# Kernel optimization log

Measured on AMD Instinct MI355X. Metric: run time of the kernel, lower is better.

Reference implementation:

```python
import jax, jax.numpy as jnp
import numpy as np

B, T, N = 64, 128, 64   # batch, win_size, input_size (= node_num)
H, E, K, CS = 64, 128, 7, 8  # hidden_size, embed_size, kernel_size, control_size
NEG_SLOPE = 0.2


def _p(key, shape, scale=0.05):
    return scale * jax.random.normal(key, shape, dtype=jnp.float32)


def setup_inputs() -> dict:
    key = jax.random.key(0)
    ks = jax.random.split(key, 32)
    inp = {
        "x": jax.random.normal(ks[0], (B, T, N), dtype=jnp.float32),
        "y": jax.random.normal(ks[1], (B, T, CS), dtype=jnp.float32),
        # Conv1d(N -> N, kernel K)
        "conv_w": _p(ks[2], (N, N, K)),
        "conv_b": _p(ks[3], (N,)),
        # rnn_enc GRU: input N -> hidden H
        "We_ih": _p(ks[4], (3 * H, N)), "We_hh": _p(ks[5], (3 * H, H)),
        "be_ih": _p(ks[6], (3 * H,)), "be_hh": _p(ks[7], (3 * H,)),
        # MP_GAT linears
        "Ww": _p(ks[8], (E, 2 * T)), "bw": _p(ks[9], (E,)),
        "Wa": _p(ks[10], (1, E)), "ba": _p(ks[11], (1,)),
        # encoder GRU: input H+N -> H
        "Wm_ih": _p(ks[12], (3 * H, H + N)), "Wm_hh": _p(ks[13], (3 * H, H)),
        "bm_ih": _p(ks[14], (3 * H,)), "bm_hh": _p(ks[15], (3 * H,)),
        # rnn_dec GRU: input H -> H
        "Wd_ih": _p(ks[16], (3 * H, H)), "Wd_hh": _p(ks[17], (3 * H, H)),
        "bd_ih": _p(ks[18], (3 * H,)), "bd_hh": _p(ks[19], (3 * H,)),
        # fc_dec: H -> N
        "W_dec": _p(ks[20], (N, H)), "b_dec": _p(ks[21], (N,)),
        # fc_pred: Linear(H,N), ReLU, Linear(N,N)
        "W_p1": _p(ks[22], (N, H)), "b_p1": _p(ks[23], (N,)),
        "W_p2": _p(ks[24], (N, N)), "b_p2": _p(ks[25], (N,)),
    }
    return inp


def gru_seq(x_seq, Wih, Whh, bih, bhh):
    """torch nn.GRU (batch_first, h0=0). x_seq: [B,T,in] -> [B,T,H]."""
    gi = jnp.einsum('bti,gi->btg', x_seq, Wih) + bih  # [B,T,3H] (precompute input proj)
    h0 = jnp.zeros((x_seq.shape[0], Whh.shape[1]), x_seq.dtype)

    def step(h, gi_t):
        gh = h @ Whh.T + bhh
        i_r, i_z, i_n = jnp.split(gi_t, 3, axis=-1)
        h_r, h_z, h_n = jnp.split(gh, 3, axis=-1)
        r = jax.nn.sigmoid(i_r + h_r)
        z = jax.nn.sigmoid(i_z + h_z)
        n = jnp.tanh(i_n + r * h_n)
        h_new = (1.0 - z) * n + z * h
        return h_new, h_new

    _, hs = jax.lax.scan(step, h0, jnp.swapaxes(gi, 0, 1))
    return jnp.swapaxes(hs, 0, 1)


def _forward(x, y, conv_w, conv_b, We_ih, We_hh, be_ih, be_hh, Ww, bw, Wa, ba,
             Wm_ih, Wm_hh, bm_ih, bm_hh, Wd_ih, Wd_hh, bd_ih, bd_hh,
             W_dec, b_dec, W_p1, b_p1, W_p2, b_p2):
    # ---- CNN: pad 'same' + Conv1d + SELU. x: [B,T,N] -> channels first [B,N,T]
    pad = (K - 1) // 2
    xc = jnp.swapaxes(x, 1, 2)
    c = jax.lax.conv_general_dilated(xc, conv_w, (1,), [(pad, pad)],
                                     dimension_numbers=('NCH', 'OIH', 'NCH'))
    c = jax.nn.selu(c + conv_b[None, :, None])  # [B,N,T]
    c_btn = jnp.swapaxes(c, 1, 2)               # [B,T,N]

    # ---- rnn_enc GRU over time
    h_out = gru_seq(c_btn, We_ih, We_hh, be_ih, be_hh)  # [B,T,H]

    # ---- MP_GAT on c (v: [B, node, seq] = [B,N,T])
    v = c
    vi = jnp.broadcast_to(v[:, :, None, :], (B, N, N, T))
    vj = jnp.broadcast_to(v[:, None, :, :], (B, N, N, T))
    v_cat = jnp.concatenate([vi, vj], axis=-1)          # [B,N,N,2T]
    x_w = jax.nn.leaky_relu(jnp.einsum('bijt,et->bije', v_cat, Ww) + bw, NEG_SLOPE)
    e = (jnp.einsum('bije,oe->bijo', x_w, Wa) + ba)[..., 0]  # [B,N,N]
    attention = jax.nn.softmax(e, axis=2)
    # dropout is identity in eval mode
    h_mp = jax.nn.sigmoid(jnp.einsum('bij,bjt->bit', attention, v))  # [B,N,T]
    h_mp = jnp.swapaxes(h_mp, 1, 2)                      # [B,T,N]

    # ---- encoder / decoder GRUs (dropout = identity in eval)
    h_cat = jnp.concatenate([h_out, h_mp], axis=2)       # [B,T,H+N]
    h_enc = gru_seq(h_cat, Wm_ih, Wm_hh, bm_ih, bm_hh)
    h_dec = gru_seq(h_enc, Wd_ih, Wd_hh, bd_ih, bd_hh)

    recon = h_dec @ W_dec.T + b_dec                      # [B,T,N]
    p = jax.nn.relu(h_dec[:, 0, :] @ W_p1.T + b_p1)
    pred = p @ W_p2.T + b_p2                             # [B,N]
    return recon, pred


def reference(x, y, conv_w, conv_b, We_ih, We_hh, be_ih, be_hh, Ww, bw, Wa, ba,
              Wm_ih, Wm_hh, bm_ih, bm_hh, Wd_ih, Wd_hh, bd_ih, bd_hh,
              W_dec, b_dec, W_p1, b_p1, W_p2, b_p2):
    return _forward(x, y, conv_w, conv_b, We_ih, We_hh, be_ih, be_hh, Ww, bw, Wa, ba,
                    Wm_ih, Wm_hh, bm_ih, bm_hh, Wd_ih, Wd_hh, bd_ih, bd_hh,
                    W_dec, b_dec, W_p1, b_p1, W_p2, b_p2)
```

## Files before the change

### kernel.cpp

```cpp
#include <hip/hip_runtime.h>
#include <math.h>

#define BB 64
#define TT 128
#define NN 64
#define HH 64
#define EE 128
#define KK 7
#define GG 192

typedef _Float16 half2_t __attribute__((ext_vector_type(2)));

__device__ __forceinline__ float sigmoidf_(float x){ return 1.f/(1.f+expf(-x)); }
__device__ __forceinline__ float fsig_(float x){
  return __builtin_amdgcn_rcpf(1.f + __builtin_amdgcn_exp2f(-1.44269504f * x));
}
__device__ __forceinline__ float ftanh_(float x){
  return fmaf(-2.f, __builtin_amdgcn_rcpf(1.f + __builtin_amdgcn_exp2f(2.88539008f * x)), 1.f);
}

#define PIPE_BARRIER() asm volatile("s_waitcnt lgkmcnt(0)\ns_barrier" ::: "memory")
#define LGKM0() asm volatile("s_waitcnt lgkmcnt(0)" ::: "memory")

__device__ __forceinline__ void loadrow_(float* d, const float* src){
  const float4* p = (const float4*)src;
  #pragma unroll
  for (int i = 0; i < 16; ++i) {
    float4 v = p[i];
    d[4*i] = v.x; d[4*i+1] = v.y; d[4*i+2] = v.z; d[4*i+3] = v.w;
  }
}
__device__ __forceinline__ void loadroww_(half2_t* d, const float* src){
  const float4* p = (const float4*)src;
  #pragma unroll
  for (int i = 0; i < 16; ++i) {
    float4 v = p[i];
    d[2*i]   = half2_t{(_Float16)v.x, (_Float16)v.y};
    d[2*i+1] = half2_t{(_Float16)v.z, (_Float16)v.w};
  }
}
__device__ __forceinline__ void mv6_(const _Float16* xs, const _Float16* ys,
    const half2_t* wxa, const half2_t* wxb, const half2_t* wxc,
    const half2_t* wya, const half2_t* wyb, const half2_t* wyc,
    float& a0, float& a1, float& a2, float& r0, float& r1, float& r2){
  const float4* x4 = (const float4*)xs;
  const float4* y4 = (const float4*)ys;
  #pragma unroll
  for (int ch = 0; ch < 8; ++ch) {
    float4 xv = x4[ch], yv = y4[ch];
    const half2_t* xq = (const half2_t*)&xv;
    const half2_t* yq = (const half2_t*)&yv;
    #pragma unroll
    for (int k = 0; k < 4; ++k) {
      int i = 4 * ch + k;
      a0 = __builtin_amdgcn_fdot2(xq[k], wxa[i], a0, false);
      a1 = __builtin_amdgcn_fdot2(xq[k], wxb[i], a1, false);
      a2 = __builtin_amdgcn_fdot2(xq[k], wxc[i], a2, false);
      r0 = __builtin_amdgcn_fdot2(yq[k], wya[i], r0, false);
      r1 = __builtin_amdgcn_fdot2(yq[k], wyb[i], r1, false);
      r2 = __builtin_amdgcn_fdot2(yq[k], wyc[i], r2, false);
    }
  }
}
__device__ __forceinline__ void mv3_(const _Float16* xs,
    const half2_t* wxa, const half2_t* wxb, const half2_t* wxc,
    float& a0, float& a1, float& a2){
  const float4* x4 = (const float4*)xs;
  #pragma unroll
  for (int ch = 0; ch < 8; ++ch) {
    float4 xv = x4[ch];
    const half2_t* xq = (const half2_t*)&xv;
    #pragma unroll
    for (int k = 0; k < 4; ++k) {
      int i = 4 * ch + k;
      a0 = __builtin_amdgcn_fdot2(xq[k], wxa[i], a0, false);
      a1 = __builtin_amdgcn_fdot2(xq[k], wxb[i], a1, false);
      a2 = __builtin_amdgcn_fdot2(xq[k], wxc[i], a2, false);
    }
  }
}

__global__ void conv_selu_kernel(const float* __restrict__ x, const float* __restrict__ w,
                                 const float* __restrict__ bias,
                                 float* __restrict__ c_nt, float* __restrict__ c_btn) {
  const int og = blockIdx.x, b = blockIdx.y, t = threadIdx.x;
  const int o0 = og * 8;
  __shared__ __align__(16) float xs[NN][TT + 1];
  __shared__ __align__(16) float ws[NN * KK][8];
  for (int idx = t; idx < TT * NN; idx += 128) {
    int tt = idx >> 6, nn = idx & 63;
    xs[nn][tt] = x[(size_t)(b * TT + tt) * NN + nn];
  }
  for (int idx = t; idx < NN * KK * 8; idx += 128) {
    int oo = idx & 7, ik = idx >> 3;
    ws[ik][oo] = w[(size_t)(o0 + oo) * (NN * KK) + ik];
  }
  __syncthreads();
  float acc[8];
  #pragma unroll
  for (int oo = 0; oo < 8; ++oo) acc[oo] = bias[o0 + oo];
  for (int i = 0; i < NN; ++i) {
    #pragma unroll
    for (int k = 0; k < KK; ++k) {
      int tt = t + k - 3;
      if (tt >= 0 && tt < TT) {
        float xv = xs[i][tt];
        const float* wp = &ws[i * KK + k][0];
        float4 w0 = *(const float4*)wp;
        float4 w1 = *(const float4*)(wp + 4);
        acc[0] += xv * w0.x; acc[1] += xv * w0.y; acc[2] += xv * w0.z; acc[3] += xv * w0.w;
        acc[4] += xv * w1.x; acc[5] += xv * w1.y; acc[6] += xv * w1.z; acc[7] += xv * w1.w;
      }
    }
  }
  const float alpha = 1.6732632423543772f, scale = 1.0507009873554805f;
  #pragma unroll
  for (int oo = 0; oo < 8; ++oo) {
    float a = acc[oo];
    float r = a > 0.f ? scale * a : scale * alpha * expm1f(a);
    int o = o0 + oo;
    c_nt[((size_t)b * NN + o) * TT + t] = r;
    c_btn[((size_t)b * TT + t) * NN + o] = r;
  }
}

__global__ void s12_kernel(const float* __restrict__ c_nt, const float* __restrict__ Ww,
                           float* __restrict__ s1, float* __restrict__ s2) {
  const int m0 = blockIdx.x * 16, col = threadIdx.x;
  __shared__ __align__(16) float ins[16][TT];
  for (int idx = col; idx < 16 * TT; idx += 128) {
    int r = idx >> 7, k = idx & 127;
    ins[r][k] = c_nt[(size_t)(m0 + r) * TT + k];
  }
  __syncthreads();
  const float* w1 = Ww + (size_t)col * (2 * TT);
  const float* w2 = w1 + TT;
  float acc1[16], acc2[16];
  #pragma unroll
  for (int r = 0; r < 16; ++r) { acc1[r] = 0.f; acc2[r] = 0.f; }
  #pragma unroll 2
  for (int k = 0; k < TT; k += 4) {
    float4 wv1 = *(const float4*)(w1 + k);
    float4 wv2 = *(const float4*)(w2 + k);
    #pragma unroll
    for (int r = 0; r < 16; ++r) {
      float4 iv = *(const float4*)&ins[r][k];
      acc1[r] += iv.x * wv1.x + iv.y * wv1.y + iv.z * wv1.z + iv.w * wv1.w;
      acc2[r] += iv.x * wv2.x + iv.y * wv2.y + iv.z * wv2.z + iv.w * wv2.w;
    }
  }
  #pragma unroll
  for (int r = 0; r < 16; ++r) {
    s1[(size_t)(m0 + r) * EE + col] = acc1[r];
    s2[(size_t)(m0 + r) * EE + col] = acc2[r];
  }
}

__global__ void gat_kernel(const float* __restrict__ s1, const float* __restrict__ s2,
                           const float* __restrict__ bw, const float* __restrict__ Wa,
                           const float* __restrict__ ba, const float* __restrict__ c_nt,
                           float* __restrict__ hmp) {
  const int it = blockIdx.x, b = blockIdx.y, tid = threadIdx.x;
  const int i0 = it * 16;
  __shared__ float s2s[NN][EE + 1];
  __shared__ float s1b[16][EE];
  __shared__ float cs[NN][TT + 1];
  __shared__ float was[EE];
  __shared__ float att[16][NN];
  for (int idx = tid; idx < NN * EE; idx += 256) {
    int j = idx >> 7, e = idx & 127;
    s2s[j][e] = s2[((size_t)b * NN + j) * EE + e] + bw[e];
  }
  for (int idx = tid; idx < 16 * EE; idx += 256) {
    int r = idx >> 7, e = idx & 127;
    s1b[r][e] = s1[((size_t)b * NN + i0 + r) * EE + e];
  }
  for (int idx = tid; idx < NN * TT; idx += 256) {
    int j = idx >> 7, t = idx & 127;
    cs[j][t] = c_nt[((size_t)b * NN + j) * TT + t];
  }
  if (tid < EE) was[tid] = Wa[tid];
  __syncthreads();
  const int wv = tid >> 6, j = tid & 63;
  #pragma unroll
  for (int pass = 0; pass < 4; ++pass) {
    const int il = pass * 4 + wv;
    float acc = 0.f;
    #pragma unroll 8
    for (int e = 0; e < EE; ++e) {
      float v = s1b[il][e] + s2s[j][e];
      v = v > 0.f ? v : 0.2f * v;
      acc += was[e] * v;
    }
    float ej = acc + ba[0];
    float mx = ej;
    for (int off = 32; off >= 1; off >>= 1) mx = fmaxf(mx, __shfl_xor(mx, off));
    float ex = __builtin_amdgcn_exp2f(1.44269504f * (ej - mx));
    float sm = ex;
    for (int off = 32; off >= 1; off >>= 1) sm += __shfl_xor(sm, off);
    att[il][j] = ex / sm;
  }
  __syncthreads();
  for (int o = tid; o < 16 * TT; o += 256) {
    int il = o >> 7, t = o & 127;
    float acc = 0.f;
    #pragma unroll 8
    for (int jj = 0; jj < NN; ++jj) acc += att[il][jj] * cs[jj][t];
    hmp[((size_t)b * TT + t) * NN + i0 + il] = sigmoidf_(acc);
  }
}

#define K4 4
__global__ __launch_bounds__(256, 1)
void fused_chain4k(const float* __restrict__ c_btn, const float* __restrict__ hmp,
                   const float* __restrict__ We_ih, const float* __restrict__ be_ih,
                   const float* __restrict__ We_hh, const float* __restrict__ be_hh,
                   const float* __restrict__ Wm_ih, const float* __restrict__ bm_ih,
                   const float* __restrict__ Wm_hh, const float* __restrict__ bm_hh,
                   const float* __restrict__ Wd_ih, const float* __restrict__ bd_ih,
                   const float* __restrict__ Wd_hh, const float* __restrict__ bd_hh,
                   const float* __restrict__ W_dec, const float* __restrict__ b_dec,
                   const float* __restrict__ W_p1, const float* __restrict__ b_p1,
                   const float* __restrict__ W_p2, const float* __restrict__ b_p2,
                   float* __restrict__ recon, float* __restrict__ pred) {
  const int b = blockIdx.x, tid = threadIdx.x, wid = tid >> 6, g = tid & 63;
  __shared__ __align__(16) _Float16 cbuf[2][K4][HH], mbuf[2][K4][HH];
  __shared__ __align__(16) _Float16 h1h[2][K4][HH], h2h[2][K4][HH], h3h[2][K4][HH];
  __shared__ __align__(16) float q2[2][K4][GG], h3f[2][K4][HH];
  __shared__ __align__(16) float h0s[HH], ps[HH];

  {
    _Float16* z1 = &h1h[0][0][0];
    _Float16* z2 = &h2h[0][0][0];
    _Float16* z3 = &h3h[0][0][0];
    _Float16* z4 = &cbuf[0][0][0];
    _Float16* z5 = &mbuf[0][0][0];
    for (int idx = tid; idx < 2 * K4 * HH; idx += 256) {
      z1[idx] = (_Float16)0.f; z2[idx] = (_Float16)0.f; z3[idx] = (_Float16)0.f;
      z4[idx] = (_Float16)0.f; z5[idx] = (_Float16)0.f;
    }
    float* zf = &h3f[0][0][0];
    for (int idx = tid; idx < 2 * K4 * HH; idx += 256) zf[idx] = 0.f;
    float* zq = &q2[0][0][0];
    for (int idx = tid; idx < 2 * K4 * GG; idx += 256) zq[idx] = 0.f;
  }

  half2_t wxa[32], wxb[32], wxc[32];
  half2_t wya[32], wyb[32], wyc[32];
  float wdec[64];
  float b0 = 0.f, b1 = 0.f, b2 = 0.f, e0 = 0.f, e1 = 0.f, e2 = 0.f, bdc = 0.f;
  if (wid == 0) {
    loadroww_(wxa, We_ih + (size_t)g * HH);
    loadroww_(wxb, We_ih + (size_t)(g + 64) * HH);
    loadroww_(wxc, We_ih + (size_t)(g + 128) * HH);
    loadroww_(wya, We_hh + (size_t)g * HH);
    loadroww_(wyb, We_hh + (size_t)(g + 64) * HH);
    loadroww_(wyc, We_hh + (size_t)(g + 128) * HH);
    b0 = be_ih[g]; b1 = be_ih[64 + g]; b2 = be_ih[128 + g];
    e0 = be_hh[g]; e1 = be_hh[64 + g]; e2 = be_hh[128 + g];
  } else if (wid == 1) {
    loadroww_(wxa, Wm_ih + (size_t)g * 128);
    loadroww_(wxb, Wm_ih + (size_t)(g + 64) * 128);
    loadroww_(wxc, Wm_ih + (size_t)(g + 128) * 128);
    loadroww_(wya, Wm_ih + (size_t)g * 128 + 64);
    loadroww_(wyb, Wm_ih + (size_t)(g + 64) * 128 + 64);
    loadroww_(wyc, Wm_ih + (size_t)(g + 128) * 128 + 64);
    b0 = bm_ih[g]; b1 = bm_ih[64 + g]; b2 = bm_ih[128 + g];
  } else if (wid == 2) {
    loadroww_(wxa, Wm_hh + (size_t)g * HH);
    loadroww_(wxb, Wm_hh + (size_t)(g + 64) * HH);
    loadroww_(wxc, Wm_hh + (size_t)(g + 128) * HH);
    loadrow_(wdec, W_dec + (size_t)g * HH);
    b0 = bm_hh[g]; b1 = bm_hh[64 + g]; b2 = bm_hh[128 + g];
    bdc = b_dec[g];
  } else {
    loadroww_(wxa, Wd_ih + (size_t)g * HH);
    loadroww_(wxb, Wd_ih + (size_t)(g + 64) * HH);
    loadroww_(wxc, Wd_ih + (size_t)(g + 128) * HH);
    loadroww_(wya, Wd_hh + (size_t)g * HH);
    loadroww_(wyb, Wd_hh + (size_t)(g + 64) * HH);
    loadroww_(wyc, Wd_hh + (size_t)(g + 128) * HH);
    b0 = bd_ih[g]; b1 = bd_ih[64 + g]; b2 = bd_ih[128 + g];
    e0 = bd_hh[g]; e1 = bd_hh[64 + g]; e2 = bd_hh[128 + g];
  }
  const float* cb = c_btn + (size_t)b * TT * NN + g;
  const float* hm = hmp   + (size_t)b * TT * NN + g;
  float cur[K4], nxt[K4];
  #pragma unroll
  for (int s = 0; s < K4; ++s) { cur[s] = 0.f; nxt[s] = 0.f; }
  if (wid == 0) {
    #pragma unroll
    for (int s = 0; s < K4; ++s) cur[s] = cb[(size_t)s * NN];
  }
  if (wid == 1) {
    #pragma unroll
    for (int s = 0; s < K4; ++s) cur[s] = hm[(size_t)s * NN];
  }
  float hown = 0.f;
  __syncthreads();

  const int NPH = TT / K4 + 4;
  for (int p = 0; p < NPH; ++p) {
    const int pw = p & 1, pr = pw ^ 1;
    if (wid == 0) {
      if (p <= TT / K4 - 1) {
        const int t0 = p * K4;
        #pragma unroll
        for (int s = 0; s < K4; ++s) cbuf[pw][s][g] = (_Float16)cur[s];
        #pragma unroll
        for (int s = 0; s < K4; ++s)
          nxt[s] = (t0 + K4 + s < TT) ? cb[(size_t)(t0 + K4 + s) * NN] : 0.f;
        #pragma unroll
        for (int s = 0; s < K4; ++s) {
          const _Float16* hp = (s == 0) ? &h1h[pr][K4-1][0] : &h1h[pw][s-1][0];
          LGKM0();
          float a0 = b0, a1 = b1, a2 = b2, r0 = e0, r1 = e1, r2 = e2;
          mv6_(&cbuf[pw][s][0], hp, wxa, wxb, wxc, wya, wyb, wyc, a0, a1, a2, r0, r1, r2);
          float r = fsig_(a0 + r0), z = fsig_(a1 + r1), n = ftanh_(a2 + r * r2);
          hown = fmaf(z, hown - n, n);
          h1h[pw][s][g] = (_Float16)hown;
        }
        #pragma unroll
        for (int s = 0; s < K4; ++s) cur[s] = nxt[s];
      }
    } else if (wid == 1) {
      if (p >= 1 && p <= TT / K4) {
        const int t0 = p * K4;
        #pragma unroll
        for (int s = 0; s < K4; ++s) mbuf[pw][s][g] = (_Float16)cur[s];
        #pragma unroll
        for (int s = 0; s < K4; ++s)
          nxt[s] = (t0 + s < TT) ? hm[(size_t)(t0 + s) * NN] : 0.f;
        LGKM0();
        #pragma unroll
        for (int s = 0; s < K4; ++s) {
          float a0 = b0, a1 = b1, a2 = b2, r0 = 0.f, r1 = 0.f, r2 = 0.f;
          mv6_(&h1h[pr][s][0], &mbuf[pw][s][0], wxa, wxb, wxc, wya, wyb, wyc,
               a0, a1, a2, r0, r1, r2);
          q2[pw][s][g] = a0 + r0; q2[pw][s][64 + g] = a1 + r1; q2[pw][s][128 + g] = a2 + r2;
        }
        #pragma unroll
        for (int s = 0; s < K4; ++s) cur[s] = nxt[s];
      }
    } else if (wid == 2) {
      if (p >= 2 && p <= TT / K4 + 1) {
        #pragma unroll
        for (int s = 0; s < K4; ++s) {
          const _Float16* hp = (s == 0) ? &h2h[pr][K4-1][0] : &h2h[pw][s-1][0];
          LGKM0();
          float a0 = b0, a1 = b1, a2 = b2;
          mv3_(hp, wxa, wxb, wxc, a0, a1, a2);
          float r = fsig_(q2[pr][s][g] + a0), z = fsig_(q2[pr][s][64 + g] + a1);
          float n = ftanh_(q2[pr][s][128 + g] + r * a2);
          hown = fmaf(z, hown - n, n);
          h2h[pw][s][g] = (_Float16)hown;
        }
      }
      if (p >= 4) {
        #pragma unroll
        for (int s = 0; s < K4; ++s) {
          int t4 = (p - 4) * K4 + s;
          const float4* h4 = (const float4*)&h3f[pr][s][0];
          float a0 = bdc, a1 = 0.f;
          #pragma unroll
          for (int i = 0; i < 8; ++i) {
            float4 hv = h4[2 * i], hw = h4[2 * i + 1];
            a0 = fmaf(hv.x, wdec[8*i],   fmaf(hv.y, wdec[8*i+1], fmaf(hv.z, wdec[8*i+2], fmaf(hv.w, wdec[8*i+3], a0))));
            a1 = fmaf(hw.x, wdec[8*i+4], fmaf(hw.y, wdec[8*i+5], fmaf(hw.z, wdec[8*i+6], fmaf(hw.w, wdec[8*i+7], a1))));
          }
          recon[((size_t)b * TT + t4) * NN + g] = a0 + a1;
        }
      }
    } else {
      if (p >= 3 && p <= TT / K4 + 2) {
        const int t0 = (p - 3) * K4;
        #pragma unroll
        for (int s = 0; s < K4; ++s) {
          const _Float16* op = (s == 0) ? &h3h[pr][K4-1][0] : &h3h[pw][s-1][0];
          LGKM0();
          float a0 = b0, a1 = b1, a2 = b2, r0 = e0, r1 = e1, r2 = e2;
          mv6_(&h2h[pr][s][0], op, wxa, wxb, wxc, wya, wyb, wyc, a0, a1, a2, r0, r1, r2);
          float r = fsig_(a0 + r0), z = fsig_(a1 + r1), n = ftanh_(a2 + r * r2);
          hown = fmaf(z, hown - n, n);
          h3h[pw][s][g] = (_Float16)hown;
          h3f[pw][s][g] = hown;
          if (t0 + s == 0) h0s[g] = hown;
        }
      }
    }
    PIPE_BARRIER();
  }

  if (wid == 2) {
    float w1r[64]; loadrow_(w1r, W_p1 + (size_t)g * HH);
    const float4* h4 = (const float4*)&h0s[0];
    float a = b_p1[g];
    #pragma unroll
    for (int i = 0; i < 16; ++i) {
      float4 hv = h4[i];
      a = fmaf(hv.x, w1r[4*i], fmaf(hv.y, w1r[4*i+1], fmaf(hv.z, w1r[4*i+2], fmaf(hv.w, w1r[4*i+3], a))));
    }
    ps[g] = fmaxf(a, 0.f);
    LGKM0();
    float w2r[64]; loadrow_(w2r, W_p2 + (size_t)g * HH);
    const float4* p4 = (const float4*)&ps[0];
    float c2 = b_p2[g];
    #pragma unroll
    for (int i = 0; i < 16; ++i) {
      float4 pv = p4[i];
      c2 = fmaf(pv.x, w2r[4*i], fmaf(pv.y, w2r[4*i+1], fmaf(pv.z, w2r[4*i+2], fmaf(pv.w, w2r[4*i+3], c2))));
    }
    pred[(size_t)b * NN + g] = c2;
  }
}

extern "C" void kernel_launch(void* const* d_in, const int* in_sizes, int n_in,
                              void* d_out, int out_size, void* d_ws, size_t ws_size,
                              hipStream_t stream) {
  const float* x      = (const float*)d_in[0];
  const float* conv_w = (const float*)d_in[2];
  const float* conv_b = (const float*)d_in[3];
  const float* We_ih  = (const float*)d_in[4];
  const float* We_hh  = (const float*)d_in[5];
  const float* be_ih  = (const float*)d_in[6];
  const float* be_hh  = (const float*)d_in[7];
  const float* Ww     = (const float*)d_in[8];
  const float* bw     = (const float*)d_in[9];
  const float* Wa     = (const float*)d_in[10];
  const float* ba     = (const float*)d_in[11];
  const float* Wm_ih  = (const float*)d_in[12];
  const float* Wm_hh  = (const float*)d_in[13];
  const float* bm_ih  = (const float*)d_in[14];
  const float* bm_hh  = (const float*)d_in[15];
  const float* Wd_ih  = (const float*)d_in[16];
  const float* Wd_hh  = (const float*)d_in[17];
  const float* bd_ih  = (const float*)d_in[18];
  const float* bd_hh  = (const float*)d_in[19];
  const float* W_dec  = (const float*)d_in[20];
  const float* b_dec  = (const float*)d_in[21];
  const float* W_p1   = (const float*)d_in[22];
  const float* b_p1   = (const float*)d_in[23];
  const float* W_p2   = (const float*)d_in[24];
  const float* b_p2   = (const float*)d_in[25];
  float* out = (float*)d_out;

  float* wsf   = (float*)d_ws;
  float* c_nt  = wsf;
  float* c_btn = c_nt  + 524288;
  float* s1    = c_btn + 524288;
  float* s2    = s1    + 524288;
  float* hmp   = s2    + 524288;

  conv_selu_kernel<<<dim3(8, BB), 128, 0, stream>>>(x, conv_w, conv_b, c_nt, c_btn);
  s12_kernel<<<BB * NN / 16, 128, 0, stream>>>(c_nt, Ww, s1, s2);
  gat_kernel<<<dim3(4, BB), 256, 0, stream>>>(s1, s2, bw, Wa, ba, c_nt, hmp);
  fused_chain4k<<<BB, 256, 0, stream>>>(c_btn, hmp,
                                        We_ih, be_ih, We_hh, be_hh,
                                        Wm_ih, bm_ih, Wm_hh, bm_hh,
                                        Wd_ih, bd_ih, Wd_hh, bd_hh,
                                        W_dec, b_dec, W_p1, b_p1, W_p2, b_p2,
                                        out, out + BB * TT * NN);
}
```

Before: 209.7 us.

## Fuse s12 projection into conv kernel and process two batches per GRU block

The s1/s2 linear projection is folded into the conv+SELU kernel, using the just-computed 8-channel tile kept in shared memory. This removes one launch and the re-read of c_nt. The fused GRU chain kernel now handles two batch elements per block with 32 blocks. Each warp interleaves two independent recurrences, which gives more instruction-level parallelism to hide latency on the serial chain, at the cost of halving the block count and doubling per-step work.

```diff
diff --git a/kernel.cpp b/kernel.cpp
--- a/kernel.cpp
+++ b/kernel.cpp
@@ -80,13 +80,15 @@
   }
 }
 
-__global__ void conv_selu_kernel(const float* __restrict__ x, const float* __restrict__ w,
-                                 const float* __restrict__ bias,
-                                 float* __restrict__ c_nt, float* __restrict__ c_btn) {
+__global__ void conv_s12_kernel(const float* __restrict__ x, const float* __restrict__ w,
+                                const float* __restrict__ bias, const float* __restrict__ Ww,
+                                float* __restrict__ c_nt, float* __restrict__ c_btn,
+                                float* __restrict__ s1, float* __restrict__ s2) {
   const int og = blockIdx.x, b = blockIdx.y, t = threadIdx.x;
   const int o0 = og * 8;
   __shared__ __align__(16) float xs[NN][TT + 1];
   __shared__ __align__(16) float ws[NN * KK][8];
+  __shared__ __align__(16) float cs[8][TT];
   for (int idx = t; idx < TT * NN; idx += 128) {
     int tt = idx >> 6, nn = idx & 63;
     xs[nn][tt] = x[(size_t)(b * TT + tt) * NN + nn];
@@ -121,38 +123,29 @@
     int o = o0 + oo;
     c_nt[((size_t)b * NN + o) * TT + t] = r;
     c_btn[((size_t)b * TT + t) * NN + o] = r;
-  }
-}
-
-__global__ void s12_kernel(const float* __restrict__ c_nt, const float* __restrict__ Ww,
-                           float* __restrict__ s1, float* __restrict__ s2) {
-  const int m0 = blockIdx.x * 16, col = threadIdx.x;
-  __shared__ __align__(16) float ins[16][TT];
-  for (int idx = col; idx < 16 * TT; idx += 128) {
-    int r = idx >> 7, k = idx & 127;
-    ins[r][k] = c_nt[(size_t)(m0 + r) * TT + k];
+    cs[oo][t] = r;
   }
   __syncthreads();
-  const float* w1 = Ww + (size_t)col * (2 * TT);
+  const float* w1 = Ww + (size_t)t * (2 * TT);
   const float* w2 = w1 + TT;
-  float acc1[16], acc2[16];
-  #pragma unroll
-  for (int r = 0; r < 16; ++r) { acc1[r] = 0.f; acc2[r] = 0.f; }
+  float a1[8], a2l[8];
+  #pragma unroll
+  for (int r = 0; r < 8; ++r) { a1[r] = 0.f; a2l[r] = 0.f; }
   #pragma unroll 2
   for (int k = 0; k < TT; k += 4) {
     float4 wv1 = *(const float4*)(w1 + k);
     float4 wv2 = *(const float4*)(w2 + k);
     #pragma unroll
-    for (int r = 0; r < 16; ++r) {
-      float4 iv = *(const float4*)&ins[r][k];
-      acc1[r] += iv.x * wv1.x + iv.y * wv1.y + iv.z * wv1.z + iv.w * wv1.w;
-      acc2[r] += iv.x * wv2.x + iv.y * wv2.y + iv.z * wv2.z + iv.w * wv2.w;
-    }
-  }
-  #pragma unroll
-  for (int r = 0; r < 16; ++r) {
-    s1[(size_t)(m0 + r) * EE + col] = acc1[r];
-    s2[(size_t)(m0 + r) * EE + col] = acc2[r];
+    for (int r = 0; r < 8; ++r) {
+      float4 cv = *(const float4*)&cs[r][k];
+      a1[r]  += cv.x * wv1.x + cv.y * wv1.y + cv.z * wv1.z + cv.w * wv1.w;
+      a2l[r] += cv.x * wv2.x + cv.y * wv2.y + cv.z * wv2.z + cv.w * wv2.w;
+    }
+  }
+  #pragma unroll
+  for (int r = 0; r < 8; ++r) {
+    s1[((size_t)b * NN + o0 + r) * EE + t] = a1[r];
+    s2[((size_t)b * NN + o0 + r) * EE + t] = a2l[r];
   }
 }
 
@@ -212,37 +205,38 @@
 
 #define K4 4
 __global__ __launch_bounds__(256, 1)
-void fused_chain4k(const float* __restrict__ c_btn, const float* __restrict__ hmp,
-                   const float* __restrict__ We_ih, const float* __restrict__ be_ih,
-                   const float* __restrict__ We_hh, const float* __restrict__ be_hh,
-                   const float* __restrict__ Wm_ih, const float* __restrict__ bm_ih,
-                   const float* __restrict__ Wm_hh, const float* __restrict__ bm_hh,
-                   const float* __restrict__ Wd_ih, const float* __restrict__ bd_ih,
-                   const float* __restrict__ Wd_hh, const float* __restrict__ bd_hh,
-                   const float* __restrict__ W_dec, const float* __restrict__ b_dec,
-                   const float* __restrict__ W_p1, const float* __restrict__ b_p1,
-                   const float* __restrict__ W_p2, const float* __restrict__ b_p2,
-                   float* __restrict__ recon, float* __restrict__ pred) {
-  const int b = blockIdx.x, tid = threadIdx.x, wid = tid >> 6, g = tid & 63;
-  __shared__ __align__(16) _Float16 cbuf[2][K4][HH], mbuf[2][K4][HH];
-  __shared__ __align__(16) _Float16 h1h[2][K4][HH], h2h[2][K4][HH], h3h[2][K4][HH];
-  __shared__ __align__(16) float q2[2][K4][GG], h3f[2][K4][HH];
-  __shared__ __align__(16) float h0s[HH], ps[HH];
+void fused_chain4k2(const float* __restrict__ c_btn, const float* __restrict__ hmp,
+                    const float* __restrict__ We_ih, const float* __restrict__ be_ih,
+                    const float* __restrict__ We_hh, const float* __restrict__ be_hh,
+                    const float* __restrict__ Wm_ih, const float* __restrict__ bm_ih,
+                    const float* __restrict__ Wm_hh, const float* __restrict__ bm_hh,
+                    const float* __restrict__ Wd_ih, const float* __restrict__ bd_ih,
+                    const float* __restrict__ Wd_hh, const float* __restrict__ bd_hh,
+                    const float* __restrict__ W_dec, const float* __restrict__ b_dec,
+                    const float* __restrict__ W_p1, const float* __restrict__ b_p1,
+                    const float* __restrict__ W_p2, const float* __restrict__ b_p2,
+                    float* __restrict__ recon, float* __restrict__ pred) {
+  const int ba0 = blockIdx.x * 2, ba1 = ba0 + 1;
+  const int tid = threadIdx.x, wid = tid >> 6, g = tid & 63;
+  __shared__ __align__(16) _Float16 cbuf[2][2][K4][HH], mbuf[2][2][K4][HH];
+  __shared__ __align__(16) _Float16 h1h[2][2][K4][HH], h2h[2][2][K4][HH], h3h[2][2][K4][HH];
+  __shared__ __align__(16) float q2[2][2][K4][GG], h3f[2][2][K4][HH];
+  __shared__ __align__(16) float h0s[2][HH], ps[2][HH];
 
   {
-    _Float16* z1 = &h1h[0][0][0];
-    _Float16* z2 = &h2h[0][0][0];
-    _Float16* z3 = &h3h[0][0][0];
-    _Float16* z4 = &cbuf[0][0][0];
-    _Float16* z5 = &mbuf[0][0][0];
-    for (int idx = tid; idx < 2 * K4 * HH; idx += 256) {
+    _Float16* z1 = &h1h[0][0][0][0];
+    _Float16* z2 = &h2h[0][0][0][0];
+    _Float16* z3 = &h3h[0][0][0][0];
+    _Float16* z4 = &cbuf[0][0][0][0];
+    _Float16* z5 = &mbuf[0][0][0][0];
+    for (int idx = tid; idx < 2 * 2 * K4 * HH; idx += 256) {
       z1[idx] = (_Float16)0.f; z2[idx] = (_Float16)0.f; z3[idx] = (_Float16)0.f;
       z4[idx] = (_Float16)0.f; z5[idx] = (_Float16)0.f;
     }
-    float* zf = &h3f[0][0][0];
-    for (int idx = tid; idx < 2 * K4 * HH; idx += 256) zf[idx] = 0.f;
-    float* zq = &q2[0][0][0];
-    for (int idx = tid; idx < 2 * K4 * GG; idx += 256) zq[idx] = 0.f;
+    float* zf = &h3f[0][0][0][0];
+    for (int idx = tid; idx < 2 * 2 * K4 * HH; idx += 256) zf[idx] = 0.f;
+    float* zq = &q2[0][0][0][0];
+    for (int idx = tid; idx < 2 * 2 * K4 * GG; idx += 256) zq[idx] = 0.f;
   }
 
   half2_t wxa[32], wxb[32], wxc[32];
@@ -283,20 +277,22 @@
     b0 = bd_ih[g]; b1 = bd_ih[64 + g]; b2 = bd_ih[128 + g];
     e0 = bd_hh[g]; e1 = bd_hh[64 + g]; e2 = bd_hh[128 + g];
   }
-  const float* cb = c_btn + (size_t)b * TT * NN + g;
-  const float* hm = hmp   + (size_t)b * TT * NN + g;
-  float cur[K4], nxt[K4];
-  #pragma unroll
-  for (int s = 0; s < K4; ++s) { cur[s] = 0.f; nxt[s] = 0.f; }
+  const float* cb0 = c_btn + (size_t)ba0 * TT * NN + g;
+  const float* cb1 = c_btn + (size_t)ba1 * TT * NN + g;
+  const float* hm0 = hmp   + (size_t)ba0 * TT * NN + g;
+  const float* hm1 = hmp   + (size_t)ba1 * TT * NN + g;
+  float curA[K4], curB[K4], nxtA[K4], nxtB[K4];
+  #pragma unroll
+  for (int s = 0; s < K4; ++s) { curA[s] = 0.f; curB[s] = 0.f; nxtA[s] = 0.f; nxtB[s] = 0.f; }
   if (wid == 0) {
     #pragma unroll
-    for (int s = 0; s < K4; ++s) cur[s] = cb[(size_t)s * NN];
+    for (int s = 0; s < K4; ++s) { curA[s] = cb0[(size_t)s * NN]; curB[s] = cb1[(size_t)s * NN]; }
   }
   if (wid == 1) {
     #pragma unroll
-    for (int s = 0; s < K4; ++s) cur[s] = hm[(size_t)s * NN];
-  }
-  float hown = 0.f;
+    for (int s = 0; s < K4; ++s) { curA[s] = hm0[(size_t)s * NN]; curB[s] = hm1[(size_t)s * NN]; }
+  }
+  float hownA = 0.f, hownB = 0.f;
   __syncthreads();
 
   const int NPH = TT / K4 + 4;
@@ -306,69 +302,98 @@
       if (p <= TT / K4 - 1) {
         const int t0 = p * K4;
         #pragma unroll
-        for (int s = 0; s < K4; ++s) cbuf[pw][s][g] = (_Float16)cur[s];
-        #pragma unroll
-        for (int s = 0; s < K4; ++s)
-          nxt[s] = (t0 + K4 + s < TT) ? cb[(size_t)(t0 + K4 + s) * NN] : 0.f;
-        #pragma unroll
-        for (int s = 0; s < K4; ++s) {
-          const _Float16* hp = (s == 0) ? &h1h[pr][K4-1][0] : &h1h[pw][s-1][0];
+        for (int s = 0; s < K4; ++s) {
+          cbuf[0][pw][s][g] = (_Float16)curA[s];
+          cbuf[1][pw][s][g] = (_Float16)curB[s];
+        }
+        #pragma unroll
+        for (int s = 0; s < K4; ++s) {
+          nxtA[s] = (t0 + K4 + s < TT) ? cb0[(size_t)(t0 + K4 + s) * NN] : 0.f;
+          nxtB[s] = (t0 + K4 + s < TT) ? cb1[(size_t)(t0 + K4 + s) * NN] : 0.f;
+        }
+        #pragma unroll
+        for (int s = 0; s < K4; ++s) {
+          const _Float16* hpA = (s == 0) ? &h1h[0][pr][K4-1][0] : &h1h[0][pw][s-1][0];
+          const _Float16* hpB = (s == 0) ? &h1h[1][pr][K4-1][0] : &h1h[1][pw][s-1][0];
           LGKM0();
           float a0 = b0, a1 = b1, a2 = b2, r0 = e0, r1 = e1, r2 = e2;
-          mv6_(&cbuf[pw][s][0], hp, wxa, wxb, wxc, wya, wyb, wyc, a0, a1, a2, r0, r1, r2);
-          float r = fsig_(a0 + r0), z = fsig_(a1 + r1), n = ftanh_(a2 + r * r2);
-          hown = fmaf(z, hown - n, n);
-          h1h[pw][s][g] = (_Float16)hown;
-        }
-        #pragma unroll
-        for (int s = 0; s < K4; ++s) cur[s] = nxt[s];
+          float c0 = b0, c1 = b1, c2 = b2, s0 = e0, s1v = e1, s2v = e2;
+          mv6_(&cbuf[0][pw][s][0], hpA, wxa, wxb, wxc, wya, wyb, wyc, a0, a1, a2, r0, r1, r2);
+          mv6_(&cbuf[1][pw][s][0], hpB, wxa, wxb, wxc, wya, wyb, wyc, c0, c1, c2, s0, s1v, s2v);
+          float rA = fsig_(a0 + r0), zA = fsig_(a1 + r1), nA = ftanh_(a2 + rA * r2);
+          float rB = fsig_(c0 + s0), zB = fsig_(c1 + s1v), nB = ftanh_(c2 + rB * s2v);
+          hownA = fmaf(zA, hownA - nA, nA);
+          hownB = fmaf(zB, hownB - nB, nB);
+          h1h[0][pw][s][g] = (_Float16)hownA;
+          h1h[1][pw][s][g] = (_Float16)hownB;
+        }
+        #pragma unroll
+        for (int s = 0; s < K4; ++s) { curA[s] = nxtA[s]; curB[s] = nxtB[s]; }
       }
     } else if (wid == 1) {
       if (p >= 1 && p <= TT / K4) {
         const int t0 = p * K4;
         #pragma unroll
-        for (int s = 0; s < K4; ++s) mbuf[pw][s][g] = (_Float16)cur[s];
-        #pragma unroll
-        for (int s = 0; s < K4; ++s)
-          nxt[s] = (t0 + s < TT) ? hm[(size_t)(t0 + s) * NN] : 0.f;
+        for (int s = 0; s < K4; ++s) {
+          mbuf[0][pw][s][g] = (_Float16)curA[s];
+          mbuf[1][pw][s][g] = (_Float16)curB[s];
+        }
+        #pragma unroll
+        for (int s = 0; s < K4; ++s) {
+          nxtA[s] = (t0 + s < TT) ? hm0[(size_t)(t0 + s) * NN] : 0.f;
+          nxtB[s] = (t0 + s < TT) ? hm1[(size_t)(t0 + s) * NN] : 0.f;
+        }
         LGKM0();
         #pragma unroll
         for (int s = 0; s < K4; ++s) {
           float a0 = b0, a1 = b1, a2 = b2, r0 = 0.f, r1 = 0.f, r2 = 0.f;
-          mv6_(&h1h[pr][s][0], &mbuf[pw][s][0], wxa, wxb, wxc, wya, wyb, wyc,
+          float c0 = b0, c1 = b1, c2 = b2, s0 = 0.f, s1v = 0.f, s2v = 0.f;
+          mv6_(&h1h[0][pr][s][0], &mbuf[0][pw][s][0], wxa, wxb, wxc, wya, wyb, wyc,
                a0, a1, a2, r0, r1, r2);
-          q2[pw][s][g] = a0 + r0; q2[pw][s][64 + g] = a1 + r1; q2[pw][s][128 + g] = a2 + r2;
-        }
-        #pragma unroll
-        for (int s = 0; s < K4; ++s) cur[s] = nxt[s];
+          mv6_(&h1h[1][pr][s][0], &mbuf[1][pw][s][0], wxa, wxb, wxc, wya, wyb, wyc,
+               c0, c1, c2, s0, s1v, s2v);
+          q2[0][pw][s][g] = a0 + r0; q2[0][pw][s][64 + g] = a1 + r1; q2[0][pw][s][128 + g] = a2 + r2;
+          q2[1][pw][s][g] = c0 + s0; q2[1][pw][s][64 + g] = c1 + s1v; q2[1][pw][s][128 + g] = c2 + s2v;
+        }
+        #pragma unroll
+        for (int s = 0; s < K4; ++s) { curA[s] = nxtA[s]; curB[s] = nxtB[s]; }
       }
     } else if (wid == 2) {
       if (p >= 2 && p <= TT / K4 + 1) {
         #pragma unroll
         for (int s = 0; s < K4; ++s) {
-          const _Float16* hp = (s == 0) ? &h2h[pr][K4-1][0] : &h2h[pw][s-1][0];
+          const _Float16* hpA = (s == 0) ? &h2h[0][pr][K4-1][0] : &h2h[0][pw][s-1][0];
+          const _Float16* hpB = (s == 0) ? &h2h[1][pr][K4-1][0] : &h2h[1][pw][s-1][0];
           LGKM0();
-          float a0 = b0, a1 = b1, a2 = b2;
-          mv3_(hp, wxa, wxb, wxc, a0, a1, a2);
-          float r = fsig_(q2[pr][s][g] + a0), z = fsig_(q2[pr][s][64 + g] + a1);
-          float n = ftanh_(q2[pr][s][128 + g] + r * a2);
-          hown = fmaf(z, hown - n, n);
-          h2h[pw][s][g] = (_Float16)hown;
+          float a0 = b0, a1 = b1, a2 = b2, c0 = b0, c1 = b1, c2 = b2;
+          mv3_(hpA, wxa, wxb, wxc, a0, a1, a2);
+          mv3_(hpB, wxa, wxb, wxc, c0, c1, c2);
+          float rA = fsig_(q2[0][pr][s][g] + a0), zA = fsig_(q2[0][pr][s][64 + g] + a1);
+          float nA = ftanh_(q2[0][pr][s][128 + g] + rA * a2);
+          float rB = fsig_(q2[1][pr][s][g] + c0), zB = fsig_(q2[1][pr][s][64 + g] + c1);
+          float nB = ftanh_(q2[1][pr][s][128 + g] + rB * c2);
+          hownA = fmaf(zA, hownA - nA, nA);
+          hownB = fmaf(zB, hownB - nB, nB);
+          h2h[0][pw][s][g] = (_Float16)hownA;
+          h2h[1][pw][s][g] = (_Float16)hownB;
         }
       }
       if (p >= 4) {
         #pragma unroll
         for (int s = 0; s < K4; ++s) {
           int t4 = (p - 4) * K4 + s;
-          const float4* h4 = (const float4*)&h3f[pr][s][0];
-          float a0 = bdc, a1 = 0.f;
           #pragma unroll
-          for (int i = 0; i < 8; ++i) {
-            float4 hv = h4[2 * i], hw = h4[2 * i + 1];
-            a0 = fmaf(hv.x, wdec[8*i],   fmaf(hv.y, wdec[8*i+1], fmaf(hv.z, wdec[8*i+2], fmaf(hv.w, wdec[8*i+3], a0))));
-            a1 = fmaf(hw.x, wdec[8*i+4], fmaf(hw.y, wdec[8*i+5], fmaf(hw.z, wdec[8*i+6], fmaf(hw.w, wdec[8*i+7], a1))));
+          for (int bb = 0; bb < 2; ++bb) {
+            const float4* h4 = (const float4*)&h3f[bb][pr][s][0];
+            float a0 = bdc, a1 = 0.f;
+            #pragma unroll
+            for (int i = 0; i < 8; ++i) {
+              float4 hv = h4[2 * i], hw = h4[2 * i + 1];
+              a0 = fmaf(hv.x, wdec[8*i],   fmaf(hv.y, wdec[8*i+1], fmaf(hv.z, wdec[8*i+2], fmaf(hv.w, wdec[8*i+3], a0))));
+              a1 = fmaf(hw.x, wdec[8*i+4], fmaf(hw.y, wdec[8*i+5], fmaf(hw.z, wdec[8*i+6], fmaf(hw.w, wdec[8*i+7], a1))));
+            }
+            recon[((size_t)(bb ? ba1 : ba0) * TT + t4) * NN + g] = a0 + a1;
           }
-          recon[((size_t)b * TT + t4) * NN + g] = a0 + a1;
         }
       }
     } else {
@@ -376,15 +401,22 @@
         const int t0 = (p - 3) * K4;
         #pragma unroll
         for (int s = 0; s < K4; ++s) {
-          const _Float16* op = (s == 0) ? &h3h[pr][K4-1][0] : &h3h[pw][s-1][0];
+          const _Float16* opA = (s == 0) ? &h3h[0][pr][K4-1][0] : &h3h[0][pw][s-1][0];
+          const _Float16* opB = (s == 0) ? &h3h[1][pr][K4-1][0] : &h3h[1][pw][s-1][0];
           LGKM0();
           float a0 = b0, a1 = b1, a2 = b2, r0 = e0, r1 = e1, r2 = e2;
-          mv6_(&h2h[pr][s][0], op, wxa, wxb, wxc, wya, wyb, wyc, a0, a1, a2, r0, r1, r2);
-          float r = fsig_(a0 + r0), z = fsig_(a1 + r1), n = ftanh_(a2 + r * r2);
-          hown = fmaf(z, hown - n, n);
-          h3h[pw][s][g] = (_Float16)hown;
-          h3f[pw][s][g] = hown;
-          if (t0 + s == 0) h0s[g] = hown;
+          float c0 = b0, c1 = b1, c2 = b2, s0 = e0, s1v = e1, s2v = e2;
+          mv6_(&h2h[0][pr][s][0], opA, wxa, wxb, wxc, wya, wyb, wyc, a0, a1, a2, r0, r1, r2);
+          mv6_(&h2h[1][pr][s][0], opB, wxa, wxb, wxc, wya, wyb, wyc, c0, c1, c2, s0, s1v, s2v);
+          float rA = fsig_(a0 + r0), zA = fsig_(a1 + r1), nA = ftanh_(a2 + rA * r2);
+          float rB = fsig_(c0 + s0), zB = fsig_(c1 + s1v), nB = ftanh_(c2 + rB * s2v);
+          hownA = fmaf(zA, hownA - nA, nA);
+          hownB = fmaf(zB, hownB - nB, nB);
+          h3h[0][pw][s][g] = (_Float16)hownA;
+          h3h[1][pw][s][g] = (_Float16)hownB;
+          h3f[0][pw][s][g] = hownA;
+          h3f[1][pw][s][g] = hownB;
+          if (t0 + s == 0) { h0s[0][g] = hownA; h0s[1][g] = hownB; }
         }
       }
     }
@@ -393,24 +425,30 @@
 
   if (wid == 2) {
     float w1r[64]; loadrow_(w1r, W_p1 + (size_t)g * HH);
-    const float4* h4 = (const float4*)&h0s[0];
-    float a = b_p1[g];
-    #pragma unroll
-    for (int i = 0; i < 16; ++i) {
-      float4 hv = h4[i];
-      a = fmaf(hv.x, w1r[4*i], fmaf(hv.y, w1r[4*i+1], fmaf(hv.z, w1r[4*i+2], fmaf(hv.w, w1r[4*i+3], a))));
-    }
-    ps[g] = fmaxf(a, 0.f);
+    #pragma unroll
+    for (int bb = 0; bb < 2; ++bb) {
+      const float4* h4 = (const float4*)&h0s[bb][0];
+      float a = b_p1[g];
+      #pragma unroll
+      for (int i = 0; i < 16; ++i) {
+        float4 hv = h4[i];
+        a = fmaf(hv.x, w1r[4*i], fmaf(hv.y, w1r[4*i+1], fmaf(hv.z, w1r[4*i+2], fmaf(hv.w, w1r[4*i+3], a))));
+      }
+      ps[bb][g] = fmaxf(a, 0.f);
+    }
     LGKM0();
     float w2r[64]; loadrow_(w2r, W_p2 + (size_t)g * HH);
-    const float4* p4 = (const float4*)&ps[0];
-    float c2 = b_p2[g];
-    #pragma unroll
-    for (int i = 0; i < 16; ++i) {
-      float4 pv = p4[i];
-      c2 = fmaf(pv.x, w2r[4*i], fmaf(pv.y, w2r[4*i+1], fmaf(pv.z, w2r[4*i+2], fmaf(pv.w, w2r[4*i+3], c2))));
-    }
-    pred[(size_t)b * NN + g] = c2;
+    #pragma unroll
+    for (int bb = 0; bb < 2; ++bb) {
+      const float4* p4 = (const float4*)&ps[bb][0];
+      float c2 = b_p2[g];
+      #pragma unroll
+      for (int i = 0; i < 16; ++i) {
+        float4 pv = p4[i];
+        c2 = fmaf(pv.x, w2r[4*i], fmaf(pv.y, w2r[4*i+1], fmaf(pv.z, w2r[4*i+2], fmaf(pv.w, w2r[4*i+3], c2))));
+      }
+      pred[(size_t)(bb ? ba1 : ba0) * NN + g] = c2;
+    }
   }
 }
 
@@ -451,13 +489,13 @@
   float* s2    = s1    + 524288;
   float* hmp   = s2    + 524288;
 
-  conv_selu_kernel<<<dim3(8, BB), 128, 0, stream>>>(x, conv_w, conv_b, c_nt, c_btn);
-  s12_kernel<<<BB * NN / 16, 128, 0, stream>>>(c_nt, Ww, s1, s2);
+  conv_s12_kernel<<<dim3(8, BB), 128, 0, stream>>>(x, conv_w, conv_b, Ww,
+                                                   c_nt, c_btn, s1, s2);
   gat_kernel<<<dim3(4, BB), 256, 0, stream>>>(s1, s2, bw, Wa, ba, c_nt, hmp);
-  fused_chain4k<<<BB, 256, 0, stream>>>(c_btn, hmp,
-                                        We_ih, be_ih, We_hh, be_hh,
-                                        Wm_ih, bm_ih, Wm_hh, bm_hh,
-                                        Wd_ih, bd_ih, Wd_hh, bd_hh,
-                                        W_dec, b_dec, W_p1, b_p1, W_p2, b_p2,
-                                        out, out + BB * TT * NN);
-}
+  fused_chain4k2<<<BB / 2, 256, 0, stream>>>(c_btn, hmp,
+                                             We_ih, be_ih, We_hh, be_hh,
+                                             Wm_ih, bm_ih, Wm_hh, bm_hh,
+                                             Wd_ih, bd_ih, Wd_hh, bd_hh,
+                                             W_dec, b_dec, W_p1, b_p1, W_p2, b_p2,
+                                             out, out + BB * TT * NN);
+}
```

Result: slower. 300.2 us (+43.1%).
